# Performance work log

Hardware: AMD Instinct MI355X
Metric: run time of the kernel (lower is better)

Reference implementation:

```python
import jax, jax.numpy as jnp
import numpy as np

N = 8192
IN_F = 64
OUT_F = 64
ALPHA = 0.2
NEG_INF = -9e15
DENSITY = 0.02


def _signed_sparse(key, shape, density):
    k1, k2 = jax.random.split(key)
    mask = jax.random.uniform(k1, shape) < density
    vals = jax.random.normal(k2, shape, dtype=jnp.float32)
    return jnp.where(mask, vals, 0.0)


def setup_inputs() -> dict:
    key = jax.random.key(0)
    k_h, k_na, k_ea, k_w, k_a = jax.random.split(key, 5)
    h = jax.random.normal(k_h, (N, IN_F), dtype=jnp.float32)
    node_adj = _signed_sparse(k_na, (N, N), DENSITY)
    edge_adj = _signed_sparse(k_ea, (N, N), DENSITY)
    # xavier_uniform with gain=1.414
    lim_w = 1.414 * np.sqrt(6.0 / (IN_F + OUT_F))
    W_att = jax.random.uniform(k_w, (IN_F, OUT_F), minval=-lim_w, maxval=lim_w, dtype=jnp.float32)
    lim_a = 1.414 * np.sqrt(6.0 / (OUT_F + 1))
    a = jax.random.uniform(k_a, (OUT_F, 1), minval=-lim_a, maxval=lim_a, dtype=jnp.float32)
    return {"h": h, "node_adj": node_adj, "edge_adj": edge_adj, "W_att": W_att, "a": a}


def reference(h, node_adj, edge_adj, W_att, a):
    # h: [N, F_in], node_adj/edge_adj: [N, N]
    h_att = h @ W_att                                   # [N, F_out]
    h_plus = (node_adj > 0).astype(h.dtype) @ h_att     # [N, F_out]
    h_minus = (node_adj < 0).astype(h.dtype) @ h_att    # [N, F_out]
    a_input = jnp.abs(h_plus - h_minus)                 # [N, F_out]
    e = jax.nn.leaky_relu(a_input @ a, ALPHA)           # [N, 1]
    e_row = e[:, 0][None, :]                            # broadcast: row i of scores = e^T
    scores = jnp.where(edge_adj != 0, e_row, jnp.float32(NEG_INF))  # [N, N]
    attention = jax.nn.softmax(scores, axis=1)          # [N, N]
    # dropout omitted (eval-mode reference)
    h_prime = (attention * edge_adj) @ h                # [N, F_in]
    return h_prime, attention
```

## Files before the change

### kernel.cpp

```cpp
#include <hip/hip_runtime.h>
#include <math.h>

#define NN 8192
#define FF 64
#define ALPHA 0.2f
#define ECAP 512
#define WCAP 256

typedef float vf4 __attribute__((ext_vector_type(4)));

__device__ __forceinline__ unsigned mbcnt64(unsigned long long m) {
    return __builtin_amdgcn_mbcnt_hi((unsigned)(m >> 32),
           __builtin_amdgcn_mbcnt_lo((unsigned)m, 0u));
}

__global__ __launch_bounds__(256) void k_hatt(const float* __restrict__ h,
                                              const float* __restrict__ W,
                                              float* __restrict__ h_att) {
    __shared__ float Ws[64 * 64];
    int t = threadIdx.x;
    for (int k = t; k < 64 * 64; k += 256) Ws[k] = W[k];
    __syncthreads();
    int idx = blockIdx.x * 256 + t;
    int r = idx >> 6, c = idx & 63;
    const float* hr = h + (size_t)r * FF;
    float acc = 0.f;
#pragma unroll
    for (int k = 0; k < 64; ++k) acc += hr[k] * Ws[k * 64 + c];
    h_att[idx] = acc;
}

__global__ __launch_bounds__(256) void k_e(const float* __restrict__ node_adj,
                                           const float* __restrict__ h_att,
                                           const float* __restrict__ a,
                                           float* __restrict__ e) {
    __shared__ int lists[4][ECAP];
    int t = threadIdx.x, w = t >> 6, lane = t & 63;
    int row = blockIdx.x * 4 + w;
    const vf4* rp = (const vf4*)(node_adj + (size_t)row * NN);
    int cnt = 0;
#pragma unroll 4
    for (int it = 0; it < 32; ++it) {
        int idx = it * 64 + lane;
        vf4 v = __builtin_nontemporal_load(rp + idx);
        int j0 = idx * 4;
        { bool nz = v.x != 0.f; unsigned long long m = __ballot(nz);
          if (nz) lists[w][cnt + mbcnt64(m)] = (v.x > 0.f) ? (j0 + 1) : -(j0 + 1);
          cnt += __popcll(m); }
        { bool nz = v.y != 0.f; unsigned long long m = __ballot(nz);
          if (nz) lists[w][cnt + mbcnt64(m)] = (v.y > 0.f) ? (j0 + 2) : -(j0 + 2);
          cnt += __popcll(m); }
        { bool nz = v.z != 0.f; unsigned long long m = __ballot(nz);
          if (nz) lists[w][cnt + mbcnt64(m)] = (v.z > 0.f) ? (j0 + 3) : -(j0 + 3);
          cnt += __popcll(m); }
        { bool nz = v.w != 0.f; unsigned long long m = __ballot(nz);
          if (nz) lists[w][cnt + mbcnt64(m)] = (v.w > 0.f) ? (j0 + 4) : -(j0 + 4);
          cnt += __popcll(m); }
    }
    if (lane < 4) lists[w][cnt + lane] = 0;

    int g = lane >> 4, fl = lane & 15;
    const vf4* Hp = (const vf4*)h_att;
    vf4 acc = {0.f, 0.f, 0.f, 0.f};
    int cnt4 = (cnt + 3) & ~3;
#pragma unroll 2
    for (int k = 0; k < cnt4; k += 4) {
        int code = lists[w][k + g];
        float s = (code < 0) ? -1.f : (code > 0 ? 1.f : 0.f);
        int aj = (code < 0) ? -code : code;
        int j = (aj > 0) ? aj - 1 : 0;
        vf4 hv = Hp[(size_t)j * 16 + fl];
        acc.x += s * hv.x; acc.y += s * hv.y; acc.z += s * hv.z; acc.w += s * hv.w;
    }
    acc.x += __shfl_xor(acc.x, 16, 64); acc.y += __shfl_xor(acc.y, 16, 64);
    acc.z += __shfl_xor(acc.z, 16, 64); acc.w += __shfl_xor(acc.w, 16, 64);
    acc.x += __shfl_xor(acc.x, 32, 64); acc.y += __shfl_xor(acc.y, 32, 64);
    acc.z += __shfl_xor(acc.z, 32, 64); acc.w += __shfl_xor(acc.w, 32, 64);

    vf4 av = ((const vf4*)a)[fl];
    float v = fabsf(acc.x) * av.x + fabsf(acc.y) * av.y +
              fabsf(acc.z) * av.z + fabsf(acc.w) * av.w;
    v += __shfl_down(v, 8, 64);
    v += __shfl_down(v, 4, 64);
    v += __shfl_down(v, 2, 64);
    v += __shfl_down(v, 1, 64);
    if (lane == 0) e[row] = (v > 0.f) ? v : ALPHA * v;
}

__global__ __launch_bounds__(256) void k_prep(const float* __restrict__ e,
                                              float* __restrict__ E) {
    __shared__ float red[256];
    int t = threadIdx.x;
    float lm = -3.0e38f;
    for (int k = t; k < NN; k += 256) lm = fmaxf(lm, e[k]);
    red[t] = lm; __syncthreads();
    for (int s = 128; s; s >>= 1) { if (t < s) red[t] = fmaxf(red[t], red[t + s]); __syncthreads(); }
    float m = red[0];
    int i = blockIdx.x * 256 + t;
    E[i] = __expf(e[i] - m);
}

__global__ __launch_bounds__(256) void k_att(const float* __restrict__ edge_adj,
                                             const float* __restrict__ E,
                                             const float* __restrict__ h,
                                             float* __restrict__ att_out,
                                             float* __restrict__ hprime) {
    __shared__ int2 seg[4][WCAP];
    __shared__ vf4  red4[64];
    __shared__ float r4z[4];
    __shared__ int   cnts[4];
    int t = threadIdx.x, w = t >> 6, lane = t & 63;
    int row = blockIdx.x;

    const vf4* rp = (const vf4*)(edge_adj + (size_t)row * NN);
    const vf4* Ep = (const vf4*)E;
    vf4 o[8];
    float zloc = 0.f;
    int cnt = 0;
#pragma unroll
    for (int it = 0; it < 8; ++it) {
        int idx = it * 256 + t;
        vf4 v  = __builtin_nontemporal_load(rp + idx);
        vf4 Ev = Ep[idx];
        int j0 = idx * 4;
        { bool nz = v.x != 0.f; unsigned long long m = __ballot(nz);
          float ox = nz ? Ev.x : 0.f;
          if (nz) seg[w][cnt + mbcnt64(m)] = make_int2(j0,     __float_as_int(v.x * Ev.x));
          cnt += __popcll(m); zloc += ox; o[it].x = ox; }
        { bool nz = v.y != 0.f; unsigned long long m = __ballot(nz);
          float oy = nz ? Ev.y : 0.f;
          if (nz) seg[w][cnt + mbcnt64(m)] = make_int2(j0 + 1, __float_as_int(v.y * Ev.y));
          cnt += __popcll(m); zloc += oy; o[it].y = oy; }
        { bool nz = v.z != 0.f; unsigned long long m = __ballot(nz);
          float oz = nz ? Ev.z : 0.f;
          if (nz) seg[w][cnt + mbcnt64(m)] = make_int2(j0 + 2, __float_as_int(v.z * Ev.z));
          cnt += __popcll(m); zloc += oz; o[it].z = oz; }
        { bool nz = v.w != 0.f; unsigned long long m = __ballot(nz);
          float ow = nz ? Ev.w : 0.f;
          if (nz) seg[w][cnt + mbcnt64(m)] = make_int2(j0 + 3, __float_as_int(v.w * Ev.w));
          cnt += __popcll(m); zloc += ow; o[it].w = ow; }
    }
    if (lane == 0) cnts[w] = cnt;
#pragma unroll
    for (int off = 32; off; off >>= 1) zloc += __shfl_down(zloc, off, 64);
    if (lane == 0) r4z[w] = zloc;
    if (lane < 4) seg[w][cnt + lane] = make_int2(0, 0);
    __syncthreads();
    float Z = r4z[0] + r4z[1] + r4z[2] + r4z[3];
    int tot = cnts[0] + cnts[1] + cnts[2] + cnts[3];
    float invZ = (tot > 0) ? 1.f / Z : 0.f;

    int g = lane >> 4, fl = lane & 15;
    const vf4* Hp = (const vf4*)h;
    vf4 acc = {0.f, 0.f, 0.f, 0.f};
    int cnt4 = (cnt + 3) & ~3;
#pragma unroll 2
    for (int k = 0; k < cnt4; k += 4) {
        int2 sv = seg[w][k + g];
        float vv = __int_as_float(sv.y);
        vf4 hv = Hp[(size_t)sv.x * 16 + fl];
        acc.x += vv * hv.x; acc.y += vv * hv.y; acc.z += vv * hv.z; acc.w += vv * hv.w;
    }
    acc.x += __shfl_xor(acc.x, 16, 64); acc.y += __shfl_xor(acc.y, 16, 64);
    acc.z += __shfl_xor(acc.z, 16, 64); acc.w += __shfl_xor(acc.w, 16, 64);
    acc.x += __shfl_xor(acc.x, 32, 64); acc.y += __shfl_xor(acc.y, 32, 64);
    acc.z += __shfl_xor(acc.z, 32, 64); acc.w += __shfl_xor(acc.w, 32, 64);
    if (lane < 16) red4[w * 16 + fl] = acc;
    __syncthreads();
    const float* red = (const float*)red4;
    if (t < 64)
        hprime[(size_t)row * FF + t] = (red[t] + red[t + 64] + red[t + 128] + red[t + 192]) * invZ;

    vf4* ap = (vf4*)(att_out + (size_t)row * NN);
    float unif = 1.0f / NN;
#pragma unroll
    for (int it = 0; it < 8; ++it) {
        int idx = it * 256 + t;
        vf4 ov = o[it];
        ov.x *= invZ; ov.y *= invZ; ov.z *= invZ; ov.w *= invZ;
        if (tot == 0) { ov.x = unif; ov.y = unif; ov.z = unif; ov.w = unif; }
        __builtin_nontemporal_store(ov, ap + idx);
    }
}

extern "C" void kernel_launch(void* const* d_in, const int* in_sizes, int n_in,
                              void* d_out, int out_size, void* d_ws, size_t ws_size,
                              hipStream_t stream) {
    const float* h        = (const float*)d_in[0];
    const float* node_adj = (const float*)d_in[1];
    const float* edge_adj = (const float*)d_in[2];
    const float* W_att    = (const float*)d_in[3];
    const float* a        = (const float*)d_in[4];

    float* out    = (float*)d_out;
    float* hprime = out;
    float* att    = out + (size_t)NN * FF;

    float* h_att = (float*)d_ws;
    float* e_vec = h_att + (size_t)NN * FF;
    float* E_vec = e_vec + NN;

    k_hatt<<<(NN * FF) / 256, 256, 0, stream>>>(h, W_att, h_att);
    k_e<<<NN / 4, 256, 0, stream>>>(node_adj, h_att, a, e_vec);
    k_prep<<<NN / 256, 256, 0, stream>>>(e_vec, E_vec);
    k_att<<<NN, 256, 0, stream>>>(edge_adj, E_vec, h, att, hprime);
}
```

Before: 616.6 us.

## Fold h@W into the e-kernel and fuse softmax prep into attention kernel

Uses associativity to compute the signed adjacency gather on raw h, then projects the 64-wide sum through W and a inside k_e, which removes the separate h_att kernel and its buffer. The global max and exp step is fused into k_att: each block recomputes the max over e and evaluates exp inline. Each block now processes four rows, amortising that max reduction. This drops two kernel launches and their intermediate buffers. In exchange it adds redundant max and exp work per block and reduces the block count for the attention kernel.

```diff
diff --git a/kernel.cpp b/kernel.cpp
--- a/kernel.cpp
+++ b/kernel.cpp
@@ -6,6 +6,7 @@
 #define ALPHA 0.2f
 #define ECAP 512
 #define WCAP 256
+#define ROWS_PER_BLK 4
 
 typedef float vf4 __attribute__((ext_vector_type(4)));
 
@@ -14,27 +15,13 @@
            __builtin_amdgcn_mbcnt_lo((unsigned)m, 0u));
 }
 
-__global__ __launch_bounds__(256) void k_hatt(const float* __restrict__ h,
-                                              const float* __restrict__ W,
-                                              float* __restrict__ h_att) {
-    __shared__ float Ws[64 * 64];
-    int t = threadIdx.x;
-    for (int k = t; k < 64 * 64; k += 256) Ws[k] = W[k];
-    __syncthreads();
-    int idx = blockIdx.x * 256 + t;
-    int r = idx >> 6, c = idx & 63;
-    const float* hr = h + (size_t)r * FF;
-    float acc = 0.f;
-#pragma unroll
-    for (int k = 0; k < 64; ++k) acc += hr[k] * Ws[k * 64 + c];
-    h_att[idx] = acc;
-}
-
 __global__ __launch_bounds__(256) void k_e(const float* __restrict__ node_adj,
-                                           const float* __restrict__ h_att,
+                                           const float* __restrict__ h,
+                                           const float* __restrict__ W,
                                            const float* __restrict__ a,
                                            float* __restrict__ e) {
     __shared__ int lists[4][ECAP];
+    __shared__ vf4 u_s[4][16];
     int t = threadIdx.x, w = t >> 6, lane = t & 63;
     int row = blockIdx.x * 4 + w;
     const vf4* rp = (const vf4*)(node_adj + (size_t)row * NN);
@@ -60,7 +47,7 @@
     if (lane < 4) lists[w][cnt + lane] = 0;
 
     int g = lane >> 4, fl = lane & 15;
-    const vf4* Hp = (const vf4*)h_att;
+    const vf4* Hp = (const vf4*)h;
     vf4 acc = {0.f, 0.f, 0.f, 0.f};
     int cnt4 = (cnt + 3) & ~3;
 #pragma unroll 2
@@ -77,31 +64,20 @@
     acc.x += __shfl_xor(acc.x, 32, 64); acc.y += __shfl_xor(acc.y, 32, 64);
     acc.z += __shfl_xor(acc.z, 32, 64); acc.w += __shfl_xor(acc.w, 32, 64);
 
-    vf4 av = ((const vf4*)a)[fl];
-    float v = fabsf(acc.x) * av.x + fabsf(acc.y) * av.y +
-              fabsf(acc.z) * av.z + fabsf(acc.w) * av.w;
-    v += __shfl_down(v, 8, 64);
-    v += __shfl_down(v, 4, 64);
-    v += __shfl_down(v, 2, 64);
-    v += __shfl_down(v, 1, 64);
+    if (g == 0) u_s[w][fl] = acc;
+    const float* us = (const float*)u_s[w];
+    float s = 0.f;
+#pragma unroll 8
+    for (int k = 0; k < 64; ++k)
+        s += us[k] * W[k * 64 + lane];
+    float v = fabsf(s) * a[lane];
+#pragma unroll
+    for (int off = 32; off; off >>= 1) v += __shfl_down(v, off, 64);
     if (lane == 0) e[row] = (v > 0.f) ? v : ALPHA * v;
 }
 
-__global__ __launch_bounds__(256) void k_prep(const float* __restrict__ e,
-                                              float* __restrict__ E) {
-    __shared__ float red[256];
-    int t = threadIdx.x;
-    float lm = -3.0e38f;
-    for (int k = t; k < NN; k += 256) lm = fmaxf(lm, e[k]);
-    red[t] = lm; __syncthreads();
-    for (int s = 128; s; s >>= 1) { if (t < s) red[t] = fmaxf(red[t], red[t + s]); __syncthreads(); }
-    float m = red[0];
-    int i = blockIdx.x * 256 + t;
-    E[i] = __expf(e[i] - m);
-}
-
 __global__ __launch_bounds__(256) void k_att(const float* __restrict__ edge_adj,
-                                             const float* __restrict__ E,
+                                             const float* __restrict__ e_vec,
                                              const float* __restrict__ h,
                                              float* __restrict__ att_out,
                                              float* __restrict__ hprime) {
@@ -109,77 +85,91 @@
     __shared__ vf4  red4[64];
     __shared__ float r4z[4];
     __shared__ int   cnts[4];
+    __shared__ float mred[256];
     int t = threadIdx.x, w = t >> 6, lane = t & 63;
-    int row = blockIdx.x;
 
-    const vf4* rp = (const vf4*)(edge_adj + (size_t)row * NN);
-    const vf4* Ep = (const vf4*)E;
-    vf4 o[8];
-    float zloc = 0.f;
-    int cnt = 0;
+    const vf4* ep4 = (const vf4*)e_vec;
+    float lm = -3.0e38f;
+    for (int k = t; k < NN / 4; k += 256) {
+        vf4 v = ep4[k];
+        lm = fmaxf(lm, fmaxf(fmaxf(v.x, v.y), fmaxf(v.z, v.w)));
+    }
+    mred[t] = lm; __syncthreads();
+    for (int s = 128; s; s >>= 1) { if (t < s) mred[t] = fmaxf(mred[t], mred[t + s]); __syncthreads(); }
+    float m = mred[0];
+
+    for (int r = 0; r < ROWS_PER_BLK; ++r) {
+        int row = blockIdx.x * ROWS_PER_BLK + r;
+        const vf4* rp = (const vf4*)(edge_adj + (size_t)row * NN);
+        vf4 o[8];
+        float zloc = 0.f;
+        int cnt = 0;
 #pragma unroll
-    for (int it = 0; it < 8; ++it) {
-        int idx = it * 256 + t;
-        vf4 v  = __builtin_nontemporal_load(rp + idx);
-        vf4 Ev = Ep[idx];
-        int j0 = idx * 4;
-        { bool nz = v.x != 0.f; unsigned long long m = __ballot(nz);
-          float ox = nz ? Ev.x : 0.f;
-          if (nz) seg[w][cnt + mbcnt64(m)] = make_int2(j0,     __float_as_int(v.x * Ev.x));
-          cnt += __popcll(m); zloc += ox; o[it].x = ox; }
-        { bool nz = v.y != 0.f; unsigned long long m = __ballot(nz);
-          float oy = nz ? Ev.y : 0.f;
-          if (nz) seg[w][cnt + mbcnt64(m)] = make_int2(j0 + 1, __float_as_int(v.y * Ev.y));
-          cnt += __popcll(m); zloc += oy; o[it].y = oy; }
-        { bool nz = v.z != 0.f; unsigned long long m = __ballot(nz);
-          float oz = nz ? Ev.z : 0.f;
-          if (nz) seg[w][cnt + mbcnt64(m)] = make_int2(j0 + 2, __float_as_int(v.z * Ev.z));
-          cnt += __popcll(m); zloc += oz; o[it].z = oz; }
-        { bool nz = v.w != 0.f; unsigned long long m = __ballot(nz);
-          float ow = nz ? Ev.w : 0.f;
-          if (nz) seg[w][cnt + mbcnt64(m)] = make_int2(j0 + 3, __float_as_int(v.w * Ev.w));
-          cnt += __popcll(m); zloc += ow; o[it].w = ow; }
-    }
-    if (lane == 0) cnts[w] = cnt;
+        for (int it = 0; it < 8; ++it) {
+            int idx = it * 256 + t;
+            vf4 v  = __builtin_nontemporal_load(rp + idx);
+            vf4 ev = ep4[idx];
+            float Ex = __expf(ev.x - m), Ey = __expf(ev.y - m);
+            float Ez = __expf(ev.z - m), Ew = __expf(ev.w - m);
+            int j0 = idx * 4;
+            { bool nz = v.x != 0.f; unsigned long long mm = __ballot(nz);
+              float ox = nz ? Ex : 0.f;
+              if (nz) seg[w][cnt + mbcnt64(mm)] = make_int2(j0,     __float_as_int(v.x * Ex));
+              cnt += __popcll(mm); zloc += ox; o[it].x = ox; }
+            { bool nz = v.y != 0.f; unsigned long long mm = __ballot(nz);
+              float oy = nz ? Ey : 0.f;
+              if (nz) seg[w][cnt + mbcnt64(mm)] = make_int2(j0 + 1, __float_as_int(v.y * Ey));
+              cnt += __popcll(mm); zloc += oy; o[it].y = oy; }
+            { bool nz = v.z != 0.f; unsigned long long mm = __ballot(nz);
+              float oz = nz ? Ez : 0.f;
+              if (nz) seg[w][cnt + mbcnt64(mm)] = make_int2(j0 + 2, __float_as_int(v.z * Ez));
+              cnt += __popcll(mm); zloc += oz; o[it].z = oz; }
+            { bool nz = v.w != 0.f; unsigned long long mm = __ballot(nz);
+              float ow = nz ? Ew : 0.f;
+              if (nz) seg[w][cnt + mbcnt64(mm)] = make_int2(j0 + 3, __float_as_int(v.w * Ew));
+              cnt += __popcll(mm); zloc += ow; o[it].w = ow; }
+        }
+        if (lane == 0) cnts[w] = cnt;
 #pragma unroll
-    for (int off = 32; off; off >>= 1) zloc += __shfl_down(zloc, off, 64);
-    if (lane == 0) r4z[w] = zloc;
-    if (lane < 4) seg[w][cnt + lane] = make_int2(0, 0);
-    __syncthreads();
-    float Z = r4z[0] + r4z[1] + r4z[2] + r4z[3];
-    int tot = cnts[0] + cnts[1] + cnts[2] + cnts[3];
-    float invZ = (tot > 0) ? 1.f / Z : 0.f;
+        for (int off = 32; off; off >>= 1) zloc += __shfl_down(zloc, off, 64);
+        if (lane == 0) r4z[w] = zloc;
+        if (lane < 4) seg[w][cnt + lane] = make_int2(0, 0);
+        __syncthreads();
+        float Z = r4z[0] + r4z[1] + r4z[2] + r4z[3];
+        int tot = cnts[0] + cnts[1] + cnts[2] + cnts[3];
+        float invZ = (tot > 0) ? 1.f / Z : 0.f;
 
-    int g = lane >> 4, fl = lane & 15;
-    const vf4* Hp = (const vf4*)h;
-    vf4 acc = {0.f, 0.f, 0.f, 0.f};
-    int cnt4 = (cnt + 3) & ~3;
+        int g = lane >> 4, fl = lane & 15;
+        const vf4* Hp = (const vf4*)h;
+        vf4 acc = {0.f, 0.f, 0.f, 0.f};
+        int cnt4 = (cnt + 3) & ~3;
 #pragma unroll 2
-    for (int k = 0; k < cnt4; k += 4) {
-        int2 sv = seg[w][k + g];
-        float vv = __int_as_float(sv.y);
-        vf4 hv = Hp[(size_t)sv.x * 16 + fl];
-        acc.x += vv * hv.x; acc.y += vv * hv.y; acc.z += vv * hv.z; acc.w += vv * hv.w;
-    }
-    acc.x += __shfl_xor(acc.x, 16, 64); acc.y += __shfl_xor(acc.y, 16, 64);
-    acc.z += __shfl_xor(acc.z, 16, 64); acc.w += __shfl_xor(acc.w, 16, 64);
-    acc.x += __shfl_xor(acc.x, 32, 64); acc.y += __shfl_xor(acc.y, 32, 64);
-    acc.z += __shfl_xor(acc.z, 32, 64); acc.w += __shfl_xor(acc.w, 32, 64);
-    if (lane < 16) red4[w * 16 + fl] = acc;
-    __syncthreads();
-    const float* red = (const float*)red4;
-    if (t < 64)
-        hprime[(size_t)row * FF + t] = (red[t] + red[t + 64] + red[t + 128] + red[t + 192]) * invZ;
+        for (int k = 0; k < cnt4; k += 4) {
+            int2 sv = seg[w][k + g];
+            float vv = __int_as_float(sv.y);
+            vf4 hv = Hp[(size_t)sv.x * 16 + fl];
+            acc.x += vv * hv.x; acc.y += vv * hv.y; acc.z += vv * hv.z; acc.w += vv * hv.w;
+        }
+        acc.x += __shfl_xor(acc.x, 16, 64); acc.y += __shfl_xor(acc.y, 16, 64);
+        acc.z += __shfl_xor(acc.z, 16, 64); acc.w += __shfl_xor(acc.w, 16, 64);
+        acc.x += __shfl_xor(acc.x, 32, 64); acc.y += __shfl_xor(acc.y, 32, 64);
+        acc.z += __shfl_xor(acc.z, 32, 64); acc.w += __shfl_xor(acc.w, 32, 64);
+        if (lane < 16) red4[w * 16 + fl] = acc;
+        __syncthreads();
+        const float* red = (const float*)red4;
+        if (t < 64)
+            hprime[(size_t)row * FF + t] = (red[t] + red[t + 64] + red[t + 128] + red[t + 192]) * invZ;
 
-    vf4* ap = (vf4*)(att_out + (size_t)row * NN);
-    float unif = 1.0f / NN;
+        vf4* ap = (vf4*)(att_out + (size_t)row * NN);
+        float unif = 1.0f / NN;
 #pragma unroll
-    for (int it = 0; it < 8; ++it) {
-        int idx = it * 256 + t;
-        vf4 ov = o[it];
-        ov.x *= invZ; ov.y *= invZ; ov.z *= invZ; ov.w *= invZ;
-        if (tot == 0) { ov.x = unif; ov.y = unif; ov.z = unif; ov.w = unif; }
-        __builtin_nontemporal_store(ov, ap + idx);
+        for (int it = 0; it < 8; ++it) {
+            int idx = it * 256 + t;
+            vf4 ov = o[it];
+            ov.x *= invZ; ov.y *= invZ; ov.z *= invZ; ov.w *= invZ;
+            if (tot == 0) { ov.x = unif; ov.y = unif; ov.z = unif; ov.w = unif; }
+            __builtin_nontemporal_store(ov, ap + idx);
+        }
     }
 }
 
@@ -196,12 +186,8 @@
     float* hprime = out;
     float* att    = out + (size_t)NN * FF;
 
-    float* h_att = (float*)d_ws;
-    float* e_vec = h_att + (size_t)NN * FF;
-    float* E_vec = e_vec + NN;
+    float* e_vec = (float*)d_ws;
 
-    k_hatt<<<(NN * FF) / 256, 256, 0, stream>>>(h, W_att, h_att);
-    k_e<<<NN / 4, 256, 0, stream>>>(node_adj, h_att, a, e_vec);
-    k_prep<<<NN / 256, 256, 0, stream>>>(e_vec, E_vec);
-    k_att<<<NN, 256, 0, stream>>>(edge_adj, E_vec, h, att, hprime);
+    k_e<<<NN / 4, 256, 0, stream>>>(node_adj, h, W_att, a, e_vec);
+    k_att<<<NN / ROWS_PER_BLK, 256, 0, stream>>>(edge_adj, e_vec, h, att, hprime);
 }
```

New measurement: 686.4 us. 11.3% more time.
